# Optimization experiments

Hardware: AMD Instinct MI355X
Metric: run time of the kernel (lower is better)

Reference implementation:

```python
import jax, jax.numpy as jnp
import numpy as np

RX, RY = 8, 2
ANGLES = [0, 90]
M_DIM = N_DIM = 2048


def _make_kernel(rx=RX, ry=RY, angles=ANGLES):
    # Faithful reproduction of GuidedFilterJAX.__init__ kernel construction.
    # For angles that are multiples of 90 deg, scipy ndimage.rotate(order=2,
    # reshape=False) on a square array is exactly np.rot90.
    kernelL = []
    for A in angles:
        k = np.zeros((rx * 4 + 1, rx * 4 + 1), dtype=np.float32)
        if ry == 0:
            k[:, rx * 2] = 1.0
        else:
            k[:, rx * 2 - ry: rx * 2 + ry + 1] = 1.0
        if A % 360 != 0:
            k = np.rot90(k, (A // 90) % 4)
        k = k[rx:3 * rx + 1, rx:3 * rx + 1]
        r = int((k.sum(1) != 0).sum()) // 2 * 2
        c = int((k.sum(0) != 0).sum()) // 2 * 2
        kernelL.append(k[rx - r // 2: rx + r // 2 + 1,
                         rx - c // 2: rx + c // 2 + 1][None, None])
    C = max(kk.shape[-2] for kk in kernelL)
    R = max(kk.shape[-1] for kk in kernelL)
    out = np.zeros((len(angles), 1, C, R), dtype=np.float32)
    for i, kk in enumerate(kernelL):
        dc = (C - kk.shape[-2]) // 2
        dr = (R - kk.shape[-1]) // 2
        out[i, :, dc:dc + kk.shape[-2], dr:dr + kk.shape[-1]] = kk[0, 0]
    return out


def setup_inputs() -> dict:
    key = jax.random.key(0)
    k1, k2 = jax.random.split(key)
    X = jax.random.normal(k1, (1, 1, M_DIM, N_DIM), dtype=jnp.float32)
    y = jax.random.normal(k2, (1, 1, M_DIM, N_DIM), dtype=jnp.float32)
    kernel = jnp.asarray(_make_kernel())  # (AngleNum, 1, c, r)
    return {"X": X, "y": y, "kernel": kernel}


def _boxfilter(x, k, pc, pr):
    # zero-pad then grouped VALID conv (feature_group_count = channels = 1)
    xp = jnp.pad(x, ((0, 0), (0, 0), (pc, pc), (pr, pr)))
    return jax.lax.conv_general_dilated(xp, k, (1, 1), 'VALID',
                                        feature_group_count=x.shape[1])


def reference(X, y, kernel):
    pr, pc = kernel.shape[-1] // 2, kernel.shape[-2] // 2
    ones = jnp.ones_like(X)
    for i in range(kernel.shape[0]):  # small fixed loop over angles
        k = kernel[i:i + 1]
        Ni = _boxfilter(ones, k, pc, pr)          # normalizer (precomputed in orig)
        mean_y = _boxfilter(y, k, pc, pr) / Ni
        mean_x = _boxfilter(X, k, pc, pr) / Ni
        X = X + (mean_y - mean_x)
    return X
```

## Files before the change

### kernel.cpp

```cpp
#include <hip/hip_runtime.h>

#define W 2048
#define H 2048
#define TX 64
#define TY 32
#define DW 92
#define DH 52
#define HS 88

typedef float f4 __attribute__((ext_vector_type(4)));

__global__ __launch_bounds__(512, 8) void guided_fused(const float* __restrict__ X,
                                                       const float* __restrict__ y,
                                                       float* __restrict__ out) {
    __shared__ __align__(16) float Ds[DH * DW];
    __shared__ __align__(16) float Hs[DH * HS];

    const int tid = threadIdx.x;
    const int bx = blockIdx.x, by = blockIdx.y;
    const int i0 = by * TY, j0 = bx * TX;
    const bool interior = (bx >= 1) & (bx <= 30) & (by >= 1) & (by <= 62);
    const float R85 = 0.011764706f;

    if (interior) {
        #pragma unroll
        for (int k = 0; k < 3; ++k) {
            int c = tid + k * 512;
            if (c < DH * 22) {
                int li = c / 22, g = c - li * 22;
                int off = (i0 - 10 + li) * W + (j0 - 12) + 4 * g;
                f4 yv = *(const f4*)&y[off];
                f4 xv = *(const f4*)&X[off];
                *(f4*)&Ds[li * DW + 4 * g] = yv - xv;
            }
        }
    } else {
        #pragma unroll
        for (int k = 0; k < 3; ++k) {
            int c = tid + k * 512;
            if (c < DH * 22) {
                int li = c / 22, g = c - li * 22;
                int gi = i0 - 10 + li, gj = j0 - 12 + 4 * g;
                f4 d = {0.f, 0.f, 0.f, 0.f};
                if ((unsigned)gi < H) {
                    if (gj >= 0 && gj + 3 < W) {
                        f4 yv = *(const f4*)&y[gi * W + gj];
                        f4 xv = *(const f4*)&X[gi * W + gj];
                        d = yv - xv;
                    } else {
                        #pragma unroll
                        for (int e = 0; e < 4; ++e) {
                            int gc = gj + e;
                            if ((unsigned)gc < W) d[e] = y[gi * W + gc] - X[gi * W + gc];
                        }
                    }
                }
                *(f4*)&Ds[li * DW + 4 * g] = d;
            }
        }
    }
    __syncthreads();

    #pragma unroll
    for (int k = 0; k < 3; ++k) {
        int c = tid + k * 512;
        if (c < DH * 20) {
            int r = c / 20, g = c - r * 20;
            const f4* dp = (const f4*)&Ds[r * DW + 4 * g];
            f4 a = dp[0], b = dp[1], cc = dp[2];
            float sb123 = b.y + b.z;
            float h = b.x + sb123;
            f4 o;
            o.x = a.z + a.w + h;
            o.y = a.w + h + b.w;
            o.z = h + b.w + cc.x;
            o.w = sb123 + b.w + cc.x + cc.y;
            *(f4*)&Hs[r * HS + 4 * g] = o;
        }
    }
    __syncthreads();

    if (tid < 180) {
        int seg = tid / 20, g = tid - seg * 20;
        int v0 = seg * 4;
        const f4* hp = (const f4*)&Hs[v0 * HS + 4 * g];
        f4 r0 = hp[0], r1 = hp[22], r2 = hp[44];
        f4 s = r0 + r1 + r2;
        #pragma unroll
        for (int t = 3; t < 17; ++t) s += hp[t * 22];
        #pragma unroll
        for (int k = 0; k < 4; ++k) {
            int v = v0 + k;
            int off = (v + 8) * DW + 4 * g + 4;
            f4 d2 = *(const f4*)&Ds[off];
            if (interior) {
                d2 -= s * R85;
            } else {
                int gi = i0 + v - 2;
                if ((unsigned)gi < H) {
                    int r0c = gi - 8 > 0 ? gi - 8 : 0;
                    int r1c = gi + 8 < H - 1 ? gi + 8 : H - 1;
                    float rowsN = (float)(r1c - r0c + 1);
                    #pragma unroll
                    for (int e = 0; e < 4; ++e) {
                        int gj = j0 - 8 + 4 * g + e;
                        if ((unsigned)gj < W) {
                            int c0 = gj - 2 > 0 ? gj - 2 : 0;
                            int c1 = gj + 2 < W - 1 ? gj + 2 : W - 1;
                            d2[e] -= s[e] * __builtin_amdgcn_rcpf(rowsN * (float)(c1 - c0 + 1));
                        }
                    }
                }
            }
            *(f4*)&Ds[off] = d2;
            if (k < 3) s += hp[(k + 17) * 22] - hp[k * 22];
        }
    }
    __syncthreads();

    if (tid < 320) {
        int seg = tid / 20, g = tid - seg * 20;
        int w0 = seg * 2;
        const f4* dp = (const f4*)&Ds[(w0 + 8) * DW + 4 * g + 4];
        f4 r0 = dp[0];
        f4 s = r0 + dp[23] + dp[46] + dp[69] + dp[92];
        f4* vp = (f4*)&Hs[w0 * HS + 4 * g];
        vp[0] = s;
        s += dp[115] - r0; vp[22] = s;
    }
    __syncthreads();

    {
        int w = tid >> 4, x0 = (tid & 15) * 4;
        int gbase = (i0 + w) * W + j0 + x0;
        f4 yv = *(const f4*)&y[gbase];
        float val[20];
        const f4* vp = (const f4*)&Hs[w * HS + x0];
        #pragma unroll
        for (int q = 0; q < 5; ++q) {
            f4 tq = vp[q];
            val[q * 4 + 0] = tq.x; val[q * 4 + 1] = tq.y;
            val[q * 4 + 2] = tq.z; val[q * 4 + 3] = tq.w;
        }
        float s = 0.f;
        #pragma unroll
        for (int c = 0; c < 17; ++c) s += val[c];
        f4 d2 = *(const f4*)&Ds[(w + 10) * DW + x0 + 12];
        f4 o;
        if (interior) {
            o.x = yv.x - d2.x + s * R85;
            s += val[17] - val[0];
            o.y = yv.y - d2.y + s * R85;
            s += val[18] - val[1];
            o.z = yv.z - d2.z + s * R85;
            s += val[19] - val[2];
            o.w = yv.w - d2.w + s * R85;
        } else {
            int gi = i0 + w;
            int r0c = gi - 2 > 0 ? gi - 2 : 0;
            int r1c = gi + 2 < H - 1 ? gi + 2 : H - 1;
            float rowsN = (float)(r1c - r0c + 1);
            float res[4];
            #pragma unroll
            for (int e = 0; e < 4; ++e) {
                int gj = j0 + x0 + e;
                int c0 = gj - 8 > 0 ? gj - 8 : 0;
                int c1 = gj + 8 < W - 1 ? gj + 8 : W - 1;
                res[e] = s * __builtin_amdgcn_rcpf(rowsN * (float)(c1 - c0 + 1));
                if (e < 3) s += val[e + 17] - val[e];
            }
            o.x = yv.x - d2.x + res[0];
            o.y = yv.y - d2.y + res[1];
            o.z = yv.z - d2.z + res[2];
            o.w = yv.w - d2.w + res[3];
        }
        *(f4*)&out[gbase] = o;
    }
}

extern "C" void kernel_launch(void* const* d_in, const int* in_sizes, int n_in,
                              void* d_out, int out_size, void* d_ws, size_t ws_size,
                              hipStream_t stream) {
    const float* X = (const float*)d_in[0];
    const float* y = (const float*)d_in[1];
    float* out = (float*)d_out;

    dim3 blk(512, 1, 1);
    dim3 grd(W / TX, H / TY, 1);
    guided_fused<<<grd, blk, 0, stream>>>(X, y, out);
}
```

Baseline: 90.60 us.

## Process two row tiles per block and prefetch the second tile into registers

Each block now handles two vertically adjacent 64x32 tiles and halves the grid. The halo for the second tile is loaded into registers while the first tile's LDS box-filter stages run, which is meant to hide global memory latency behind compute. The final horizontal sum is also simplified to use vector adds in place of a 20-element scalar array. In exchange, register pressure rises from holding six f4 prefetch registers, which may hurt occupancy under launch_bounds(512,8). The grid also shrinks to 1024 blocks, reducing parallelism.

```diff
diff --git a/kernel.cpp b/kernel.cpp
--- a/kernel.cpp
+++ b/kernel.cpp
@@ -17,165 +17,185 @@
     __shared__ __align__(16) float Hs[DH * HS];
 
     const int tid = threadIdx.x;
-    const int bx = blockIdx.x, by = blockIdx.y;
-    const int i0 = by * TY, j0 = bx * TX;
-    const bool interior = (bx >= 1) & (bx <= 30) & (by >= 1) & (by <= 62);
+    const int bx = blockIdx.x, byp = blockIdx.y;
+    const int j0 = bx * TX;
+    const int i0A = (2 * byp) * TY;
+    const int i0B = i0A + TY;
+    const bool xin = (bx >= 1) & (bx <= 30);
+    const bool intA = xin & (byp >= 1);
+    const bool intB = xin & (byp <= 30);
     const float R85 = 0.011764706f;
 
-    if (interior) {
+    f4 ry[3], rx[3];
+
+    auto load_tile_regs = [&](int i0, bool interior) {
+        #pragma unroll
+        for (int k = 0; k < 3; ++k) {
+            int c = tid + k * 512;
+            ry[k] = (f4){0.f, 0.f, 0.f, 0.f};
+            rx[k] = (f4){0.f, 0.f, 0.f, 0.f};
+            if (c < DH * 22) {
+                int li = c / 22, g = c - li * 22;
+                int gi = i0 - 10 + li, gj = j0 - 12 + 4 * g;
+                if (interior) {
+                    int off = gi * W + gj;
+                    ry[k] = *(const f4*)&y[off];
+                    rx[k] = *(const f4*)&X[off];
+                } else if ((unsigned)gi < H) {
+                    if (gj >= 0 && gj + 3 < W) {
+                        ry[k] = *(const f4*)&y[gi * W + gj];
+                        rx[k] = *(const f4*)&X[gi * W + gj];
+                    } else {
+                        #pragma unroll
+                        for (int e = 0; e < 4; ++e) {
+                            int gc = gj + e;
+                            if ((unsigned)gc < W) {
+                                ry[k][e] = y[gi * W + gc];
+                                rx[k][e] = X[gi * W + gc];
+                            }
+                        }
+                    }
+                }
+            }
+        }
+    };
+
+    auto store_tile_lds = [&]() {
         #pragma unroll
         for (int k = 0; k < 3; ++k) {
             int c = tid + k * 512;
             if (c < DH * 22) {
                 int li = c / 22, g = c - li * 22;
-                int off = (i0 - 10 + li) * W + (j0 - 12) + 4 * g;
-                f4 yv = *(const f4*)&y[off];
-                f4 xv = *(const f4*)&X[off];
-                *(f4*)&Ds[li * DW + 4 * g] = yv - xv;
-            }
-        }
-    } else {
+                *(f4*)&Ds[li * DW + 4 * g] = ry[k] - rx[k];
+            }
+        }
+    };
+
+    auto compute_tile = [&](int i0, bool interior) {
         #pragma unroll
         for (int k = 0; k < 3; ++k) {
             int c = tid + k * 512;
-            if (c < DH * 22) {
-                int li = c / 22, g = c - li * 22;
-                int gi = i0 - 10 + li, gj = j0 - 12 + 4 * g;
-                f4 d = {0.f, 0.f, 0.f, 0.f};
-                if ((unsigned)gi < H) {
-                    if (gj >= 0 && gj + 3 < W) {
-                        f4 yv = *(const f4*)&y[gi * W + gj];
-                        f4 xv = *(const f4*)&X[gi * W + gj];
-                        d = yv - xv;
-                    } else {
+            if (c < DH * 20) {
+                int r = c / 20, g = c - r * 20;
+                const f4* dp = (const f4*)&Ds[r * DW + 4 * g];
+                f4 a = dp[0], b = dp[1], cc = dp[2];
+                float sb123 = b.y + b.z;
+                float h = b.x + sb123;
+                f4 o;
+                o.x = a.z + a.w + h;
+                o.y = a.w + h + b.w;
+                o.z = h + b.w + cc.x;
+                o.w = sb123 + b.w + cc.x + cc.y;
+                *(f4*)&Hs[r * HS + 4 * g] = o;
+            }
+        }
+        __syncthreads();
+
+        if (tid < 180) {
+            int seg = tid / 20, g = tid - seg * 20;
+            int v0 = seg * 4;
+            const f4* hp = (const f4*)&Hs[v0 * HS + 4 * g];
+            f4 r0 = hp[0], r1 = hp[22], r2 = hp[44];
+            f4 s = r0 + r1 + r2;
+            #pragma unroll
+            for (int t = 3; t < 17; ++t) s += hp[t * 22];
+            #pragma unroll
+            for (int k = 0; k < 4; ++k) {
+                int v = v0 + k;
+                int off = (v + 8) * DW + 4 * g + 4;
+                f4 d2 = *(const f4*)&Ds[off];
+                if (interior) {
+                    d2 -= s * R85;
+                } else {
+                    int gi = i0 + v - 2;
+                    if ((unsigned)gi < H) {
+                        int r0c = gi - 8 > 0 ? gi - 8 : 0;
+                        int r1c = gi + 8 < H - 1 ? gi + 8 : H - 1;
+                        float rowsN = (float)(r1c - r0c + 1);
                         #pragma unroll
                         for (int e = 0; e < 4; ++e) {
-                            int gc = gj + e;
-                            if ((unsigned)gc < W) d[e] = y[gi * W + gc] - X[gi * W + gc];
+                            int gj = j0 - 8 + 4 * g + e;
+                            if ((unsigned)gj < W) {
+                                int c0 = gj - 2 > 0 ? gj - 2 : 0;
+                                int c1 = gj + 2 < W - 1 ? gj + 2 : W - 1;
+                                d2[e] -= s[e] * __builtin_amdgcn_rcpf(rowsN * (float)(c1 - c0 + 1));
+                            }
                         }
                     }
                 }
-                *(f4*)&Ds[li * DW + 4 * g] = d;
-            }
-        }
-    }
+                *(f4*)&Ds[off] = d2;
+                if (k < 3) s += hp[(k + 17) * 22] - hp[k * 22];
+            }
+        }
+        __syncthreads();
+
+        if (tid < 320) {
+            int seg = tid / 20, g = tid - seg * 20;
+            int w0 = seg * 2;
+            const f4* dp = (const f4*)&Ds[(w0 + 8) * DW + 4 * g + 4];
+            f4 r0 = dp[0];
+            f4 s = r0 + dp[23] + dp[46] + dp[69] + dp[92];
+            f4* vp = (f4*)&Hs[w0 * HS + 4 * g];
+            vp[0] = s;
+            s += dp[115] - r0; vp[22] = s;
+        }
+        __syncthreads();
+
+        {
+            int w = tid >> 4, x0 = (tid & 15) * 4;
+            int gbase = (i0 + w) * W + j0 + x0;
+            f4 yv = *(const f4*)&y[gbase];
+            const f4* vp = (const f4*)&Hs[w * HS + x0];
+            f4 v0 = vp[0], v4 = vp[4];
+            f4 t = v0 + vp[1] + vp[2] + vp[3];
+            float s = t.x + t.y + t.z + t.w + v4.x;
+            f4 d2 = *(const f4*)&Ds[(w + 10) * DW + x0 + 12];
+            f4 o;
+            if (interior) {
+                o.x = yv.x - d2.x + s * R85;
+                s += v4.y - v0.x;
+                o.y = yv.y - d2.y + s * R85;
+                s += v4.z - v0.y;
+                o.z = yv.z - d2.z + s * R85;
+                s += v4.w - v0.z;
+                o.w = yv.w - d2.w + s * R85;
+            } else {
+                int gi = i0 + w;
+                int r0c = gi - 2 > 0 ? gi - 2 : 0;
+                int r1c = gi + 2 < H - 1 ? gi + 2 : H - 1;
+                float rowsN = (float)(r1c - r0c + 1);
+                float sl0 = v4.y - v0.x, sl1 = v4.z - v0.y, sl2 = v4.w - v0.z;
+                float res[4];
+                #pragma unroll
+                for (int e = 0; e < 4; ++e) {
+                    int gj = j0 + x0 + e;
+                    int c0 = gj - 8 > 0 ? gj - 8 : 0;
+                    int c1 = gj + 8 < W - 1 ? gj + 8 : W - 1;
+                    res[e] = s * __builtin_amdgcn_rcpf(rowsN * (float)(c1 - c0 + 1));
+                    if (e == 0) s += sl0;
+                    if (e == 1) s += sl1;
+                    if (e == 2) s += sl2;
+                }
+                o.x = yv.x - d2.x + res[0];
+                o.y = yv.y - d2.y + res[1];
+                o.z = yv.z - d2.z + res[2];
+                o.w = yv.w - d2.w + res[3];
+            }
+            *(f4*)&out[gbase] = o;
+        }
+    };
+
+    load_tile_regs(i0A, intA);
+    store_tile_lds();
     __syncthreads();
 
-    #pragma unroll
-    for (int k = 0; k < 3; ++k) {
-        int c = tid + k * 512;
-        if (c < DH * 20) {
-            int r = c / 20, g = c - r * 20;
-            const f4* dp = (const f4*)&Ds[r * DW + 4 * g];
-            f4 a = dp[0], b = dp[1], cc = dp[2];
-            float sb123 = b.y + b.z;
-            float h = b.x + sb123;
-            f4 o;
-            o.x = a.z + a.w + h;
-            o.y = a.w + h + b.w;
-            o.z = h + b.w + cc.x;
-            o.w = sb123 + b.w + cc.x + cc.y;
-            *(f4*)&Hs[r * HS + 4 * g] = o;
-        }
-    }
+    load_tile_regs(i0B, intB);
+    compute_tile(i0A, intA);
     __syncthreads();
 
-    if (tid < 180) {
-        int seg = tid / 20, g = tid - seg * 20;
-        int v0 = seg * 4;
-        const f4* hp = (const f4*)&Hs[v0 * HS + 4 * g];
-        f4 r0 = hp[0], r1 = hp[22], r2 = hp[44];
-        f4 s = r0 + r1 + r2;
-        #pragma unroll
-        for (int t = 3; t < 17; ++t) s += hp[t * 22];
-        #pragma unroll
-        for (int k = 0; k < 4; ++k) {
-            int v = v0 + k;
-            int off = (v + 8) * DW + 4 * g + 4;
-            f4 d2 = *(const f4*)&Ds[off];
-            if (interior) {
-                d2 -= s * R85;
-            } else {
-                int gi = i0 + v - 2;
-                if ((unsigned)gi < H) {
-                    int r0c = gi - 8 > 0 ? gi - 8 : 0;
-                    int r1c = gi + 8 < H - 1 ? gi + 8 : H - 1;
-                    float rowsN = (float)(r1c - r0c + 1);
-                    #pragma unroll
-                    for (int e = 0; e < 4; ++e) {
-                        int gj = j0 - 8 + 4 * g + e;
-                        if ((unsigned)gj < W) {
-                            int c0 = gj - 2 > 0 ? gj - 2 : 0;
-                            int c1 = gj + 2 < W - 1 ? gj + 2 : W - 1;
-                            d2[e] -= s[e] * __builtin_amdgcn_rcpf(rowsN * (float)(c1 - c0 + 1));
-                        }
-                    }
-                }
-            }
-            *(f4*)&Ds[off] = d2;
-            if (k < 3) s += hp[(k + 17) * 22] - hp[k * 22];
-        }
-    }
+    store_tile_lds();
     __syncthreads();
-
-    if (tid < 320) {
-        int seg = tid / 20, g = tid - seg * 20;
-        int w0 = seg * 2;
-        const f4* dp = (const f4*)&Ds[(w0 + 8) * DW + 4 * g + 4];
-        f4 r0 = dp[0];
-        f4 s = r0 + dp[23] + dp[46] + dp[69] + dp[92];
-        f4* vp = (f4*)&Hs[w0 * HS + 4 * g];
-        vp[0] = s;
-        s += dp[115] - r0; vp[22] = s;
-    }
-    __syncthreads();
-
-    {
-        int w = tid >> 4, x0 = (tid & 15) * 4;
-        int gbase = (i0 + w) * W + j0 + x0;
-        f4 yv = *(const f4*)&y[gbase];
-        float val[20];
-        const f4* vp = (const f4*)&Hs[w * HS + x0];
-        #pragma unroll
-        for (int q = 0; q < 5; ++q) {
-            f4 tq = vp[q];
-            val[q * 4 + 0] = tq.x; val[q * 4 + 1] = tq.y;
-            val[q * 4 + 2] = tq.z; val[q * 4 + 3] = tq.w;
-        }
-        float s = 0.f;
-        #pragma unroll
-        for (int c = 0; c < 17; ++c) s += val[c];
-        f4 d2 = *(const f4*)&Ds[(w + 10) * DW + x0 + 12];
-        f4 o;
-        if (interior) {
-            o.x = yv.x - d2.x + s * R85;
-            s += val[17] - val[0];
-            o.y = yv.y - d2.y + s * R85;
-            s += val[18] - val[1];
-            o.z = yv.z - d2.z + s * R85;
-            s += val[19] - val[2];
-            o.w = yv.w - d2.w + s * R85;
-        } else {
-            int gi = i0 + w;
-            int r0c = gi - 2 > 0 ? gi - 2 : 0;
-            int r1c = gi + 2 < H - 1 ? gi + 2 : H - 1;
-            float rowsN = (float)(r1c - r0c + 1);
-            float res[4];
-            #pragma unroll
-            for (int e = 0; e < 4; ++e) {
-                int gj = j0 + x0 + e;
-                int c0 = gj - 8 > 0 ? gj - 8 : 0;
-                int c1 = gj + 8 < W - 1 ? gj + 8 : W - 1;
-                res[e] = s * __builtin_amdgcn_rcpf(rowsN * (float)(c1 - c0 + 1));
-                if (e < 3) s += val[e + 17] - val[e];
-            }
-            o.x = yv.x - d2.x + res[0];
-            o.y = yv.y - d2.y + res[1];
-            o.z = yv.z - d2.z + res[2];
-            o.w = yv.w - d2.w + res[3];
-        }
-        *(f4*)&out[gbase] = o;
-    }
+    compute_tile(i0B, intB);
 }
 
 extern "C" void kernel_launch(void* const* d_in, const int* in_sizes, int n_in,
@@ -186,6 +206,6 @@
     float* out = (float*)d_out;
 
     dim3 blk(512, 1, 1);
-    dim3 grd(W / TX, H / TY, 1);
+    dim3 grd(W / TX, H / (2 * TY), 1);
     guided_fused<<<grd, blk, 0, stream>>>(X, y, out);
 }
```

Result: slower. 95.00 us (+4.9%).
